# Kernel tuning notes

Measured on AMD Instinct MI355X. Metric: run time of the kernel, lower is better.

Reference implementation:

```python
import jax, jax.numpy as jnp
import numpy as np

B, C_IN, N = 128, 256, 1024
C_OUT = 256
L = 3069  # 3 * (N - 1) triplet indices, multiple of kernel_size=3


def setup_inputs() -> dict:
    key = jax.random.key(0)
    k1, k2, k3, k4 = jax.random.split(key, 4)
    data = jax.random.normal(k1, (B, C_IN, N), dtype=jnp.float32)
    indexes = jax.random.randint(k2, (B, L, 1), 0, N, dtype=jnp.int64)
    # Conv1d(in_dims, out_dims, kernel_size=3) params, PyTorch layout [out, in, k]
    fan_in = C_IN * 3
    bound = 1.0 / np.sqrt(fan_in)
    weight = jax.random.uniform(k3, (C_OUT, C_IN, 3), dtype=jnp.float32, minval=-bound, maxval=bound)
    bias = jax.random.uniform(k4, (C_OUT,), dtype=jnp.float32, minval=-bound, maxval=bound)
    return {"data": data, "indexes": indexes, "weight": weight, "bias": bias}


def reference(data, indexes, weight, bias):
    # gather: data[b, c, indexes[b, l, 0]] -> [B, C_IN, L]
    idx = indexes[:, :, 0]  # [B, L]
    gathered = jnp.take_along_axis(data, idx[:, None, :], axis=2)  # broadcast over channel dim
    # Conv1d kernel_size=3 stride=3 == per-triplet matmul:
    # reshape [B, C_IN, L] -> [B, C_IN, L//3, 3]; contract with weight [C_OUT, C_IN, 3]
    trip = gathered.reshape(B, gathered.shape[1], L // 3, 3)
    feats = jnp.einsum('bcnk,ock->bon', trip, weight) + bias[None, :, None]  # [B, C_OUT, L//3]
    # prepend a zero column (padding slot for node index 0)
    zeros = jnp.zeros((feats.shape[0], feats.shape[1], 1), dtype=feats.dtype)
    feats = jnp.concatenate((zeros, feats), axis=2)  # [B, C_OUT, L//3 + 1]
    return (feats, indexes)
```

## Files before the change

### kernel.cpp

```cpp
#include <hip/hip_runtime.h>

#define B_      128
#define C_IN_   256
#define NPTS    1024
#define C_OUT_  256
#define L_      3069
#define NTRIP   1023
#define T_OUT   1024
#define FEATS_SIZE (B_ * C_OUT_ * T_OUT)
#define KTOT    768

#define THREADS 512

typedef __attribute__((ext_vector_type(8))) short           bf16x8;
typedef __attribute__((ext_vector_type(8))) unsigned short  ushort8;
typedef __attribute__((ext_vector_type(4))) unsigned short  ushort4v;
typedef __attribute__((ext_vector_type(4))) float           f32x4;

__device__ __forceinline__ unsigned short f2bf(float f) {
    union { float f; unsigned u; } v; v.f = f;
    unsigned r = (v.u + 0x7FFFu + ((v.u >> 16) & 1u)) >> 16;
    return (unsigned short)r;
}

__device__ __forceinline__ void gload16(const void* g, void* l) {
    __builtin_amdgcn_global_load_lds(
        (const __attribute__((address_space(1))) unsigned int*)g,
        (__attribute__((address_space(3))) unsigned int*)l, 16, 0, 0);
}

#define WOFF_T  0
#define DOFF_T  393216
#define WS_NEED_T2 (393216 + 67108864)

#define NSLICE  24
#define ABYTES  16384
#define BBYTES  8192
#define BUFSZ   (ABYTES + BBYTES)
#define SMEM4   (3 * BUFSZ)
#define IDX4    (2 * BUFSZ)
#define BN2     128

__global__ __launch_bounds__(256) void convert_w4(
    const float* __restrict__ w, unsigned short* __restrict__ wbf4)
{
    int i = blockIdx.x * 256 + threadIdx.x;
    if (i >= C_OUT_ * KTOT) return;
    int e  = i & 7;
    int j  = (i >> 3) & 3;
    int r  = (i >> 5) & 255;
    int s  = i >> 13;
    int t  = s >> 3;
    int cb = s & 7;
    int lgp = j ^ (r & 3);
    int c  = cb * 32 + lgp * 8 + e;
    wbf4[i] = f2bf(w[r * KTOT + c * 3 + t]);
}

__global__ __launch_bounds__(256) void transpose_data(
    const float* __restrict__ data, unsigned short* __restrict__ dataT)
{
    __shared__ float T[64][68];
    const int bid = blockIdx.x;
    const int b   = bid >> 6;
    const int ct  = (bid & 63) >> 4;
    const int nt  = bid & 15;
    const int c0  = ct * 64, n0 = nt * 64;
    const int t   = threadIdx.x;
    const int row = t >> 2;
    const int q   = t & 3;

    const float* src = data + ((size_t)(b * C_IN_ + c0 + row)) * NPTS + n0 + q * 16;
    #pragma unroll
    for (int j = 0; j < 4; ++j) {
        float4 v = *(const float4*)(src + j * 4);
        *(float4*)&T[row][q * 16 + j * 4] = v;
    }
    __syncthreads();

    ushort8 o0, o1;
    #pragma unroll
    for (int j = 0; j < 8; ++j)  o0[j] = f2bf(T[q * 16 + j][row]);
    #pragma unroll
    for (int j = 0; j < 8; ++j)  o1[j] = f2bf(T[q * 16 + 8 + j][row]);
    unsigned short* dst = dataT + ((size_t)(b * NPTS) + n0 + row) * C_IN_ + c0 + q * 16;
    *(ushort8*)(dst)     = o0;
    *(ushort8*)(dst + 8) = o1;
}

__global__ __launch_bounds__(THREADS, 4) void treeconv_mfma4(
    const unsigned short* __restrict__ wbf4,
    const unsigned short* __restrict__ dataT,
    const int*   __restrict__ indexes,
    const float* __restrict__ bias,
    float*       __restrict__ out)
{
    __shared__ alignas(16) unsigned char smem[SMEM4];
    int* idx_s = (int*)(smem + IDX4);

    const int tid = threadIdx.x;
    const int wg  = (blockIdx.x & 7) * 128 + (blockIdx.x >> 3);
    const int b   = wg >> 3;
    const int nt0 = (wg & 7) * BN2;

    if (tid < BN2 * 3) {
        int off = nt0 * 3 + tid;
        idx_s[tid] = (off < L_) ? indexes[b * L_ + off] : 0;
    }
    __syncthreads();

    const int lane = tid & 63;
    const int wid  = tid >> 6;
    const int wm   = wid >> 1;
    const int wn   = wid & 1;
    const int l15  = lane & 15;
    const int lg   = lane >> 4;

    const int slotB = wid * 64 + lane;
    const int nB    = slotB >> 2;
    const int lgp   = (slotB & 3) ^ (nB & 3);
    const unsigned boff0 = (unsigned)(idx_s[nB * 3 + 0] * 512 + lgp * 16);
    const unsigned boff1 = (unsigned)(idx_s[nB * 3 + 1] * 512 + lgp * 16);
    const unsigned boff2 = (unsigned)(idx_s[nB * 3 + 2] * 512 + lgp * 16);
    const int bdst = ABYTES + slotB * 16;

    const char* dTb  = (const char*)dataT + (size_t)b * NPTS * C_IN_ * 2;
    const char* wsrc = (const char*)wbf4;
    const int   a0   = (wid * 128 + lane) * 16;

    const unsigned xsl   = (unsigned)((lg ^ (l15 & 3)) << 4);
    const unsigned abase = (unsigned)((wm * 64 + l15) * 64) + xsl;
    const unsigned bbase = (unsigned)(ABYTES + (wn * 64 + l15) * 64) + xsl;

    f32x4 acc[4][4];
    #pragma unroll
    for (int mi = 0; mi < 4; ++mi)
        #pragma unroll
        for (int ni = 0; ni < 4; ++ni)
            acc[mi][ni] = (f32x4){0.f, 0.f, 0.f, 0.f};

#define STAGE4(s, buf) do {                                                   \
        gload16(wsrc + (s) * ABYTES + a0,        smem + (buf) * BUFSZ + a0);  \
        gload16(wsrc + (s) * ABYTES + a0 + 1024, smem + (buf) * BUFSZ + a0 + 1024); \
        unsigned bo = (((s) >> 3) == 0 ? boff0 : ((s) >> 3) == 1 ? boff1 : boff2) \
                      + (unsigned)(((s) & 7) * 64);                           \
        gload16(dTb + bo, smem + (buf) * BUFSZ + bdst);                       \
    } while (0)

    STAGE4(0, 0);
    STAGE4(1, 1);

    #pragma unroll
    for (int s = 0; s < NSLICE; ++s) {
        if (s == NSLICE - 1) asm volatile("s_waitcnt vmcnt(0)" ::: "memory");
        else                 asm volatile("s_waitcnt vmcnt(3)" ::: "memory");
        __builtin_amdgcn_s_barrier();
        asm volatile("" ::: "memory");

        const unsigned char* bufp = smem + (s % 3) * BUFSZ;
        bf16x8 a[4], bb[4];
        #pragma unroll
        for (int mi = 0; mi < 4; ++mi)
            a[mi] = *(const bf16x8*)(bufp + abase + mi * 1024);
        #pragma unroll
        for (int ni = 0; ni < 4; ++ni)
            bb[ni] = *(const bf16x8*)(bufp + bbase + ni * 1024);

        if (s + 2 < NSLICE) STAGE4(s + 2, (s + 2) % 3);

        #pragma unroll
        for (int mi = 0; mi < 4; ++mi)
            #pragma unroll
            for (int ni = 0; ni < 4; ++ni)
                acc[mi][ni] = __builtin_amdgcn_mfma_f32_16x16x32_bf16(
                    a[mi], bb[ni], acc[mi][ni], 0, 0, 0);
    }
#undef STAGE4

    float* outB = out + (size_t)b * (C_OUT_ * T_OUT);
    #pragma unroll
    for (int mi = 0; mi < 4; ++mi) {
        #pragma unroll
        for (int r = 0; r < 4; ++r) {
            int o = wm * 64 + mi * 16 + lg * 4 + r;
            float bv = bias[o];
            #pragma unroll
            for (int ni = 0; ni < 4; ++ni) {
                int n = nt0 + wn * 64 + ni * 16 + l15;
                if (n < NTRIP)
                    outB[o * T_OUT + 1 + n] = acc[mi][ni][r] + bv;
            }
        }
    }
}

#define BN      64
#define BK      96
#define NCHUNK  8
#define AS_OFF  0
#define BS_OFF  49152
#define IDX_OFF 61440
#define SMEM_BYTES 62208

template<bool PREW>
__global__ __launch_bounds__(THREADS, 4) void treeconv_mfma(
    const float* __restrict__ data,
    const int*   __restrict__ indexes,
    const float* __restrict__ w32,
    const unsigned short* __restrict__ wbf,
    const float* __restrict__ bias,
    float*       __restrict__ out)
{
    __shared__ alignas(16) unsigned char smem[SMEM_BYTES];
    int* idx_s = (int*)(smem + IDX_OFF);

    const int tid = threadIdx.x;
    const int b   = blockIdx.x >> 4;
    const int nt0 = (blockIdx.x & 15) * BN;

    if (tid < BN * 3) {
        int off = nt0 * 3 + tid;
        idx_s[tid] = (off < L_) ? indexes[b * L_ + off] : 0;
    }
    __syncthreads();

    const int lane = tid & 63;
    const int wid  = tid >> 6;
    const int wm   = wid >> 1;
    const int wn   = wid & 1;
    const int l15  = lane & 15;
    const int lg   = lane >> 4;

    f32x4 acc[4][2];
    #pragma unroll
    for (int mi = 0; mi < 4; ++mi)
        #pragma unroll
        for (int ni = 0; ni < 2; ++ni)
            acc[mi][ni] = (f32x4){0.f, 0.f, 0.f, 0.f};

    const float* dataB = data + (size_t)b * (C_IN_ * NPTS);
    const int ar = tid >> 1;
    const int ah = tid & 1;
    const int gn = tid & 63;
    const int g8 = tid >> 6;

    for (int kc = 0; kc < NCHUNK; ++kc) {
        {
            const int ab = ar * 192 + ah * 96;
            const int sw = (ar & 7) << 4;
            if (PREW) {
                const ushort8* src = (const ushort8*)(wbf + ar * KTOT + kc * BK + ah * 48);
                #pragma unroll
                for (int j = 0; j < 6; ++j) {
                    ushort8 v = src[j];
                    *(ushort8*)(smem + ((ab + j * 16) ^ sw)) = v;
                }
            } else {
                const float* src = w32 + ar * KTOT + kc * BK + ah * 48;
                #pragma unroll
                for (int j = 0; j < 6; ++j) {
                    float4 fa = *(const float4*)(src + j * 8);
                    float4 fb = *(const float4*)(src + j * 8 + 4);
                    ushort8 v;
                    v[0] = f2bf(fa.x); v[1] = f2bf(fa.y); v[2] = f2bf(fa.z); v[3] = f2bf(fa.w);
                    v[4] = f2bf(fb.x); v[5] = f2bf(fb.y); v[6] = f2bf(fb.z); v[7] = f2bf(fb.w);
                    *(ushort8*)(smem + ((ab + j * 16) ^ sw)) = v;
                }
            }
        }
        {
            const int* ip = idx_s + gn * 3;
            int ix0 = ip[0], ix1 = ip[1], ix2 = ip[2];
            const float* dp = dataB + (kc * 32 + g8 * 4) * NPTS;
            unsigned short vals[12];
            #pragma unroll
            for (int ci = 0; ci < 4; ++ci) {
                vals[ci * 3 + 0] = f2bf(dp[ix0]);
                vals[ci * 3 + 1] = f2bf(dp[ix1]);
                vals[ci * 3 + 2] = f2bf(dp[ix2]);
                dp += NPTS;
            }
            const int bb = BS_OFF + gn * 192 + g8 * 24;
            const int sw = (gn & 7) << 4;
            #pragma unroll
            for (int q = 0; q < 3; ++q) {
                ushort4v v;
                v[0] = vals[q * 4 + 0]; v[1] = vals[q * 4 + 1];
                v[2] = vals[q * 4 + 2]; v[3] = vals[q * 4 + 3];
                *(ushort4v*)(smem + ((bb + q * 8) ^ sw)) = v;
            }
        }
        __syncthreads();

        #pragma unroll
        for (int ks = 0; ks < 3; ++ks) {
            bf16x8 a[4], bf[2];
            const int kb = ks * 64 + lg * 16;
            #pragma unroll
            for (int mi = 0; mi < 4; ++mi) {
                int row = wm * 64 + mi * 16 + l15;
                a[mi] = *(const bf16x8*)(smem + ((row * 192 + kb) ^ ((row & 7) << 4)));
            }
            #pragma unroll
            for (int ni = 0; ni < 2; ++ni) {
                int row = wn * 32 + ni * 16 + l15;
                bf[ni] = *(const bf16x8*)(smem + ((BS_OFF + row * 192 + kb) ^ ((row & 7) << 4)));
            }
            #pragma unroll
            for (int mi = 0; mi < 4; ++mi)
                #pragma unroll
                for (int ni = 0; ni < 2; ++ni)
                    acc[mi][ni] = __builtin_amdgcn_mfma_f32_16x16x32_bf16(
                        a[mi], bf[ni], acc[mi][ni], 0, 0, 0);
        }
        __syncthreads();
    }

    float* outB = out + (size_t)b * (C_OUT_ * T_OUT);
    #pragma unroll
    for (int mi = 0; mi < 4; ++mi) {
        #pragma unroll
        for (int r = 0; r < 4; ++r) {
            int o = wm * 64 + mi * 16 + lg * 4 + r;
            float bv = bias[o];
            #pragma unroll
            for (int ni = 0; ni < 2; ++ni) {
                int n = nt0 + wn * 32 + ni * 16 + l15;
                if (n < NTRIP)
                    outB[o * T_OUT + 1 + n] = acc[mi][ni][r] + bv;
            }
        }
    }
}

__global__ __launch_bounds__(256) void convert_w(
    const float* __restrict__ w, unsigned short* __restrict__ wbf)
{
    int i = (blockIdx.x * 256 + threadIdx.x) * 4;
    if (i < C_OUT_ * KTOT) {
        float4 f = *(const float4*)(w + i);
        ushort4v v;
        v[0] = f2bf(f.x); v[1] = f2bf(f.y); v[2] = f2bf(f.z); v[3] = f2bf(f.w);
        *(ushort4v*)(wbf + i) = v;
    }
}

__global__ __launch_bounds__(256) void aux_kernel(
    const int* __restrict__ indexes, float* __restrict__ out)
{
    int i = blockIdx.x * 256 + threadIdx.x;
    if (i < B_ * L_)
        out[FEATS_SIZE + i] = (float)indexes[i];
    if (i < B_ * C_OUT_)
        out[(size_t)i * T_OUT] = 0.0f;
}

extern "C" void kernel_launch(void* const* d_in, const int* in_sizes, int n_in,
                              void* d_out, int out_size, void* d_ws, size_t ws_size,
                              hipStream_t stream)
{
    const float* data    = (const float*)d_in[0];
    const int*   indexes = (const int*)d_in[1];
    const float* weight  = (const float*)d_in[2];
    const float* bias    = (const float*)d_in[3];
    float* out = (float*)d_out;

    hipLaunchKernelGGL(aux_kernel, dim3((B_ * L_ + 255) / 256), dim3(256), 0, stream,
                       indexes, out);

    if (ws_size >= (size_t)WS_NEED_T2) {
        unsigned short* wbf4  = (unsigned short*)((char*)d_ws + WOFF_T);
        unsigned short* dataT = (unsigned short*)((char*)d_ws + DOFF_T);
        hipLaunchKernelGGL(convert_w4, dim3((C_OUT_ * KTOT + 255) / 256), dim3(256),
                           0, stream, weight, wbf4);
        hipLaunchKernelGGL(transpose_data, dim3(B_ * 64), dim3(256), 0, stream,
                           data, dataT);
        hipLaunchKernelGGL(treeconv_mfma4, dim3(B_ * 8), dim3(THREADS), 0, stream,
                           wbf4, dataT, indexes, bias, out);
    } else if (ws_size >= (size_t)(C_OUT_ * KTOT * 2)) {
        unsigned short* wbf = (unsigned short*)d_ws;
        hipLaunchKernelGGL(convert_w, dim3((C_OUT_ * KTOT / 4 + 255) / 256), dim3(256),
                           0, stream, weight, wbf);
        hipLaunchKernelGGL((treeconv_mfma<true>), dim3(B_ * 16), dim3(THREADS), 0, stream,
                           data, indexes, weight, wbf, bias, out);
    } else {
        hipLaunchKernelGGL((treeconv_mfma<false>), dim3(B_ * 16), dim3(THREADS), 0, stream,
                           data, indexes, weight, (const unsigned short*)d_ws, bias, out);
    }
}
```

Before: 116.5 us.

## Load weight fragments directly into registers and deepen gathered-data LDS pipeline

```diff
diff --git a/kernel.cpp b/kernel.cpp
--- a/kernel.cpp
+++ b/kernel.cpp
@@ -34,27 +34,28 @@
 #define WS_NEED_T2 (393216 + 67108864)
 
 #define NSLICE  24
-#define ABYTES  16384
 #define BBYTES  8192
-#define BUFSZ   (ABYTES + BBYTES)
-#define SMEM4   (3 * BUFSZ)
-#define IDX4    (2 * BUFSZ)
+#define NBUF    6
+#define IDX5    (NBUF * BBYTES)
+#define SMEM5   (IDX5 + 1536)
 #define BN2     128
 
-__global__ __launch_bounds__(256) void convert_w4(
-    const float* __restrict__ w, unsigned short* __restrict__ wbf4)
+#define WAITV(n) asm volatile("s_waitcnt vmcnt(" #n ")" ::: "memory")
+#define MEMFENCE asm volatile("" ::: "memory")
+
+__global__ __launch_bounds__(256) void convert_w5(
+    const float* __restrict__ w, unsigned short* __restrict__ wbf5)
 {
     int i = blockIdx.x * 256 + threadIdx.x;
     if (i >= C_OUT_ * KTOT) return;
     int e  = i & 7;
-    int j  = (i >> 3) & 3;
+    int lg = (i >> 3) & 3;
     int r  = (i >> 5) & 255;
     int s  = i >> 13;
     int t  = s >> 3;
     int cb = s & 7;
-    int lgp = j ^ (r & 3);
-    int c  = cb * 32 + lgp * 8 + e;
-    wbf4[i] = f2bf(w[r * KTOT + c * 3 + t]);
+    int c  = cb * 32 + lg * 8 + e;
+    wbf5[i] = f2bf(w[r * KTOT + c * 3 + t]);
 }
 
 __global__ __launch_bounds__(256) void transpose_data(
@@ -88,15 +89,15 @@
     *(ushort8*)(dst + 8) = o1;
 }
 
-__global__ __launch_bounds__(THREADS, 4) void treeconv_mfma4(
-    const unsigned short* __restrict__ wbf4,
+__global__ __launch_bounds__(THREADS, 2) void treeconv_mfma5(
+    const unsigned short* __restrict__ wbf5,
     const unsigned short* __restrict__ dataT,
     const int*   __restrict__ indexes,
     const float* __restrict__ bias,
     float*       __restrict__ out)
 {
-    __shared__ alignas(16) unsigned char smem[SMEM4];
-    int* idx_s = (int*)(smem + IDX4);
+    __shared__ alignas(16) unsigned char smem[SMEM5];
+    int* idx_s = (int*)(smem + IDX5);
 
     const int tid = threadIdx.x;
     const int wg  = (blockIdx.x & 7) * 128 + (blockIdx.x >> 3);
@@ -122,15 +123,14 @@
     const unsigned boff0 = (unsigned)(idx_s[nB * 3 + 0] * 512 + lgp * 16);
     const unsigned boff1 = (unsigned)(idx_s[nB * 3 + 1] * 512 + lgp * 16);
     const unsigned boff2 = (unsigned)(idx_s[nB * 3 + 2] * 512 + lgp * 16);
-    const int bdst = ABYTES + slotB * 16;
 
     const char* dTb  = (const char*)dataT + (size_t)b * NPTS * C_IN_ * 2;
-    const char* wsrc = (const char*)wbf4;
-    const int   a0   = (wid * 128 + lane) * 16;
+    const char* wsrc = (const char*)wbf5;
+    const int   awoff = (wm * 64 + l15) * 64 + lg * 16;
+    unsigned char* bdst0 = smem + slotB * 16;
 
     const unsigned xsl   = (unsigned)((lg ^ (l15 & 3)) << 4);
-    const unsigned abase = (unsigned)((wm * 64 + l15) * 64) + xsl;
-    const unsigned bbase = (unsigned)(ABYTES + (wn * 64 + l15) * 64) + xsl;
+    const unsigned bbase = (unsigned)((wn * 64 + l15) * 64) + xsl;
 
     f32x4 acc[4][4];
     #pragma unroll
@@ -139,43 +139,59 @@
         for (int ni = 0; ni < 4; ++ni)
             acc[mi][ni] = (f32x4){0.f, 0.f, 0.f, 0.f};
 
-#define STAGE4(s, buf) do {                                                   \
-        gload16(wsrc + (s) * ABYTES + a0,        smem + (buf) * BUFSZ + a0);  \
-        gload16(wsrc + (s) * ABYTES + a0 + 1024, smem + (buf) * BUFSZ + a0 + 1024); \
-        unsigned bo = (((s) >> 3) == 0 ? boff0 : ((s) >> 3) == 1 ? boff1 : boff2) \
+#define BSTAGE(s) do {                                                        \
+        unsigned bo = ((s) < 8 ? boff0 : (s) < 16 ? boff1 : boff2)            \
                       + (unsigned)(((s) & 7) * 64);                           \
-        gload16(dTb + bo, smem + (buf) * BUFSZ + bdst);                       \
+        gload16(dTb + bo, bdst0 + ((s) % NBUF) * BBYTES);                     \
     } while (0)
 
-    STAGE4(0, 0);
-    STAGE4(1, 1);
+#define ALOAD(s, dst) do {                                                    \
+        const char* ap_ = wsrc + (s) * 16384 + awoff;                         \
+        dst[0] = *(const bf16x8*)(ap_);                                       \
+        dst[1] = *(const bf16x8*)(ap_ + 1024);                                \
+        dst[2] = *(const bf16x8*)(ap_ + 2048);                                \
+        dst[3] = *(const bf16x8*)(ap_ + 3072);                                \
+    } while (0)
+
+    bf16x8 areg[3][4];
+
+    ALOAD(0, areg[0]);
+    ALOAD(1, areg[1]);
+    MEMFENCE;
+    BSTAGE(0); BSTAGE(1); BSTAGE(2); BSTAGE(3); BSTAGE(4);
 
     #pragma unroll
     for (int s = 0; s < NSLICE; ++s) {
-        if (s == NSLICE - 1) asm volatile("s_waitcnt vmcnt(0)" ::: "memory");
-        else                 asm volatile("s_waitcnt vmcnt(3)" ::: "memory");
+        if      (s == 0)  WAITV(4);
+        else if (s == 1)  WAITV(8);
+        else if (s == 2)  WAITV(12);
+        else if (s == 3)  WAITV(16);
+        else if (s <= 19) WAITV(20);
+        else if (s == 20) WAITV(19);
+        else if (s == 21) WAITV(18);
+        else if (s == 22) WAITV(17);
+        else              WAITV(12);
         __builtin_amdgcn_s_barrier();
-        asm volatile("" ::: "memory");
-
-        const unsigned char* bufp = smem + (s % 3) * BUFSZ;
-        bf16x8 a[4], bb[4];
-        #pragma unroll
-        for (int mi = 0; mi < 4; ++mi)
-            a[mi] = *(const bf16x8*)(bufp + abase + mi * 1024);
+
+        const unsigned char* bufp = smem + (s % NBUF) * BBYTES;
+        bf16x8 bb[4];
         #pragma unroll
         for (int ni = 0; ni < 4; ++ni)
             bb[ni] = *(const bf16x8*)(bufp + bbase + ni * 1024);
 
-        if (s + 2 < NSLICE) STAGE4(s + 2, (s + 2) % 3);
+        if (s + 2 < NSLICE) ALOAD(s + 2, areg[(s + 2) % 3]);
+        MEMFENCE;
+        if (s + 5 < NSLICE) BSTAGE(s + 5);
 
         #pragma unroll
         for (int mi = 0; mi < 4; ++mi)
             #pragma unroll
             for (int ni = 0; ni < 4; ++ni)
                 acc[mi][ni] = __builtin_amdgcn_mfma_f32_16x16x32_bf16(
-                    a[mi], bb[ni], acc[mi][ni], 0, 0, 0);
-    }
-#undef STAGE4
+                    areg[s % 3][mi], bb[ni], acc[mi][ni], 0, 0, 0);
+    }
+#undef BSTAGE
+#undef ALOAD
 
     float* outB = out + (size_t)b * (C_OUT_ * T_OUT);
     #pragma unroll
@@ -369,14 +385,14 @@
                        indexes, out);
 
     if (ws_size >= (size_t)WS_NEED_T2) {
-        unsigned short* wbf4  = (unsigned short*)((char*)d_ws + WOFF_T);
+        unsigned short* wbf5  = (unsigned short*)((char*)d_ws + WOFF_T);
         unsigned short* dataT = (unsigned short*)((char*)d_ws + DOFF_T);
-        hipLaunchKernelGGL(convert_w4, dim3((C_OUT_ * KTOT + 255) / 256), dim3(256),
-                           0, stream, weight, wbf4);
+        hipLaunchKernelGGL(convert_w5, dim3((C_OUT_ * KTOT + 255) / 256), dim3(256),
+                           0, stream, weight, wbf5);
         hipLaunchKernelGGL(transpose_data, dim3(B_ * 64), dim3(256), 0, stream,
                            data, dataT);
-        hipLaunchKernelGGL(treeconv_mfma4, dim3(B_ * 8), dim3(THREADS), 0, stream,
-                           wbf4, dataT, indexes, bias, out);
+        hipLaunchKernelGGL(treeconv_mfma5, dim3(B_ * 8), dim3(THREADS), 0, stream,
+                           wbf5, dataT, indexes, bias, out);
     } else if (ws_size >= (size_t)(C_OUT_ * KTOT * 2)) {
         unsigned short* wbf = (unsigned short*)d_ws;
         hipLaunchKernelGGL(convert_w, dim3((C_OUT_ * KTOT / 4 + 255) / 256), dim3(256),
```

Result: slower. 135.9 us (+16.7%).
